# Performance work log

Hardware: AMD Instinct MI355X
Metric: run time of the kernel (lower is better)

## Reference

```python
import jax, jax.numpy as jnp
import numpy as np

NUM_FEATURES = 1024
NUM_SAMPLES = 32768
BATCH = 4096
TEMP = 0.05
EPS = 1e-12


def setup_inputs() -> dict:
    key = jax.random.key(0)
    k1, k2, k3, k4 = jax.random.split(key, 4)
    inputs = jax.random.normal(k1, (BATCH, NUM_FEATURES), dtype=jnp.float32)
    targets = jax.random.randint(k2, (BATCH,), 0, NUM_SAMPLES, dtype=jnp.int64)
    corrected_targets = jax.random.randint(k3, (BATCH,), 0, NUM_SAMPLES, dtype=jnp.int64)
    # memory bank: buffer is zeros-initialized in torch, but in practice it is
    # filled with L2-normalized cluster centroids before use; emulate that.
    feats = jax.random.normal(k4, (NUM_SAMPLES, NUM_FEATURES), dtype=jnp.float32)
    feats = feats / jnp.linalg.norm(feats, axis=1, keepdims=True)
    return {"inputs": inputs, "targets": targets,
            "corrected_targets": corrected_targets, "features": feats}


def reference(inputs, targets, corrected_targets, features):
    # F.normalize(inputs, dim=1)
    x = inputs / jnp.maximum(jnp.linalg.norm(inputs, axis=1, keepdims=True), EPS)
    # CM.forward: inputs @ features.T, then / temp
    logits = jnp.einsum('bd,nd->bn', x, features) / TEMP  # [B, N]
    # F.cross_entropy(logits, corrected_targets, reduction='mean')
    logp = jax.nn.log_softmax(logits, axis=1)
    nll = -jnp.take_along_axis(logp, corrected_targets[:, None], axis=1)[:, 0]
    return jnp.mean(nll)
```

## Files before the change

kernel.cpp:

```cpp
#include <hip/hip_runtime.h>
#include <stdint.h>

#define B_ROWS 4096
#define N_FEAT 32768
#define K_DIM  1024
#define BM 256
#define BN 256
#define NT2 (N_FEAT / BN)
#define NKT (K_DIM / 64)

typedef __attribute__((ext_vector_type(8))) short bf16x8;
typedef __attribute__((ext_vector_type(4))) float f32x4;
typedef __attribute__((address_space(1))) unsigned char ga_u8;
typedef __attribute__((address_space(3))) unsigned char lds_u8;

__device__ inline unsigned short f2bf(float f) {
  union { float f; unsigned u; } v; v.f = f;
  unsigned r = v.u + 0x7FFF + ((v.u >> 16) & 1);
  return (unsigned short)(r >> 16);
}
__device__ inline float bf2f(unsigned short u) {
  union { unsigned u; float f; } v; v.u = ((unsigned)u) << 16;
  return v.f;
}

__global__ void k_prep(const float* __restrict__ in, unsigned short* __restrict__ xbf,
                       const float* __restrict__ f, unsigned short* __restrict__ fbf) {
  int bid = blockIdx.x;
  int t = threadIdx.x;
  if (bid < B_ROWS) {
    int row = bid;
    float4 v = reinterpret_cast<const float4*>(in + (size_t)row * K_DIM)[t];
    float ssq = v.x * v.x + v.y * v.y + v.z * v.z + v.w * v.w;
    #pragma unroll
    for (int d = 1; d < 64; d <<= 1) ssq += __shfl_xor(ssq, d);
    __shared__ float sm[4];
    if ((t & 63) == 0) sm[t >> 6] = ssq;
    __syncthreads();
    float nrm = sqrtf(sm[0] + sm[1] + sm[2] + sm[3]);
    float inv = 1.0f / fmaxf(nrm, 1e-12f);
    ushort4 o;
    o.x = f2bf(v.x * inv); o.y = f2bf(v.y * inv);
    o.z = f2bf(v.z * inv); o.w = f2bf(v.w * inv);
    reinterpret_cast<ushort4*>(xbf + (size_t)row * K_DIM)[t] = o;
  } else {
    const long n4 = (long)N_FEAT * K_DIM / 4;
    long i = (long)(bid - B_ROWS) * 256 + t;
    const long stride = 2048L * 256;
    for (; i < n4; i += stride) {
      float4 v = reinterpret_cast<const float4*>(f)[i];
      ushort4 o;
      o.x = f2bf(v.x); o.y = f2bf(v.y); o.z = f2bf(v.z); o.w = f2bf(v.w);
      reinterpret_cast<ushort4*>(fbf)[i] = o;
    }
  }
}

__global__ void k_tgt(const unsigned short* __restrict__ xbf,
                      const unsigned short* __restrict__ fbf,
                      const int* __restrict__ tgt, float* __restrict__ out) {
  int row = blockIdx.x * 4 + (threadIdx.x >> 6);
  int lane = threadIdx.x & 63;
  int t = tgt[row];
  const uint4* xa = reinterpret_cast<const uint4*>(xbf + (size_t)row * K_DIM + lane * 16);
  const uint4* fa = reinterpret_cast<const uint4*>(fbf + (size_t)t * K_DIM + lane * 16);
  float s = 0.f;
  #pragma unroll
  for (int j = 0; j < 2; ++j) {
    uint4 av = xa[j], fv = fa[j];
    const unsigned* ap = &av.x;
    const unsigned* fp = &fv.x;
    #pragma unroll
    for (int q = 0; q < 4; ++q) {
      s += bf2f((unsigned short)(ap[q] & 0xffff)) * bf2f((unsigned short)(fp[q] & 0xffff));
      s += bf2f((unsigned short)(ap[q] >> 16)) * bf2f((unsigned short)(fp[q] >> 16));
    }
  }
  #pragma unroll
  for (int d = 1; d < 64; d <<= 1) s += __shfl_xor(s, d);
  if (lane == 0) out[row] = s * 20.0f;
}


#define XSTR(s) STR(s)
#define STR(s) #s
#define WAITV(N)  asm volatile("s_waitcnt vmcnt(" XSTR(N) ")" ::: "memory")
#define LGKM0     do { asm volatile("s_waitcnt lgkmcnt(0)" ::: "memory"); __builtin_amdgcn_sched_barrier(0); } while(0)
#define BAR       __builtin_amdgcn_s_barrier()
#define SCHED0    __builtin_amdgcn_sched_barrier(0)
#define PRIO1     __builtin_amdgcn_s_setprio(1)
#define PRIO0     __builtin_amdgcn_s_setprio(0)

__launch_bounds__(512, 2)
__global__ void k_gemm8(const unsigned short* __restrict__ xbf,
                        const unsigned short* __restrict__ fbf,
                        float* __restrict__ m_part, float* __restrict__ l_part) {
  __shared__ __align__(16) char lds_all[131072];
  char* ldsc = lds_all;

  int tid = threadIdx.x;
  int lane = tid & 63;
  int wid = tid >> 6;
  int wr = wid >> 2;
  int wc = wid & 3;
  int r15 = lane & 15;
  int g = lane >> 4;

  int bid = blockIdx.x;
  int swz = (bid & 7) * 256 + (bid >> 3);
  int mt = swz >> 7;
  int nt = swz & 127;
  int mBase = mt * BM, nBase = nt * BN;

  int lswz = ((g ^ ((r15 >> 1) & 3)) << 4);
  int aRow = (wr * 128 + r15) * 64 + lswz;
  int bRow = (wc * 64 + r15) * 64 + lswz + 32768;

  int stRow = wid * 32 + (lane >> 2);
  int src_cb = (((lane & 3) ^ ((lane >> 3) & 3)) << 4);
  const char* srcA = (const char*)xbf + (size_t)(mBase + stRow) * (K_DIM * 2) + src_cb;
  const char* srcB = (const char*)fbf + (size_t)(nBase + stRow) * (K_DIM * 2) + src_cb;

#define STAGE(BSEL_, MAT, KH, T) do { \
    const char* gsrc = ((MAT) ? srcB : srcA) + (T) * 128 + (KH) * 64; \
    char* ldst = ldsc + (BSEL_) * 65536 + (MAT) * 32768 + (KH) * 16384 + wid * 2048; \
    __builtin_amdgcn_global_load_lds((const ga_u8*)gsrc, (lds_u8*)ldst, 16, 0, 0); \
    __builtin_amdgcn_global_load_lds((const ga_u8*)(gsrc + 32768), (lds_u8*)(ldst + 1024), 16, 0, 0); \
  } while(0)

#define PHASE(T, KH, DOST, SB, SKH, ST, VMN) do { \
    char* bufc = ldsc + ((T) & 1) * 65536 + (KH) * 16384; \
    _Pragma("unroll") \
    for (int fm = 0; fm < 8; ++fm) \
      a[fm] = *reinterpret_cast<const bf16x8*>(bufc + aRow + fm * 1024); \
    _Pragma("unroll") \
    for (int fn = 0; fn < 4; ++fn) \
      b[fn] = *reinterpret_cast<const bf16x8*>(bufc + bRow + fn * 1024); \
    if (DOST) { STAGE(SB, 0, SKH, ST); STAGE(SB, 1, SKH, ST); } \
    WAITV(VMN); \
    BAR; LGKM0; PRIO1; \
    _Pragma("unroll") \
    for (int fm = 0; fm < 8; ++fm) \
      _Pragma("unroll") \
      for (int fn = 0; fn < 4; ++fn) \
        acc[fm][fn] = __builtin_amdgcn_mfma_f32_16x16x32_bf16(a[fm], b[fn], acc[fm][fn], 0, 0, 0); \
    PRIO0; BAR; SCHED0; \
  } while(0)

  f32x4 acc[8][4];
  #pragma unroll
  for (int i = 0; i < 8; ++i)
    #pragma unroll
    for (int j = 0; j < 4; ++j)
      acc[i][j] = (f32x4){0.f, 0.f, 0.f, 0.f};
  bf16x8 a[8], b[4];

  STAGE(0, 0, 0, 0); STAGE(0, 1, 0, 0);
  STAGE(0, 0, 1, 0); STAGE(0, 1, 1, 0);
  STAGE(1, 0, 0, 1); STAGE(1, 1, 0, 1);
  WAITV(8);
  BAR; SCHED0;

  for (int t = 0; t < NKT - 2; ++t) {
    PHASE(t, 0, 1, (t + 1) & 1, 1, t + 1, 8);
    PHASE(t, 1, 1, t & 1,       0, t + 2, 8);
  }
  PHASE(14, 0, 1, 1, 1, 15, 8);
  PHASE(14, 1, 0, 0, 0, 0, 4);
  PHASE(15, 0, 0, 0, 0, 0, 0);
  PHASE(15, 1, 0, 0, 0, 0, 0);

  asm volatile("s_waitcnt vmcnt(0) lgkmcnt(0)" ::: "memory");
  __syncthreads();
  float* sm_m = (float*)lds_all;
  float* sm_l = (float*)(lds_all + 4096);

  #pragma unroll
  for (int mf = 0; mf < 8; ++mf)
    #pragma unroll
    for (int fn = 0; fn < 4; ++fn)
      acc[mf][fn] = acc[mf][fn] * 20.0f;

  #pragma unroll
  for (int mf = 0; mf < 8; ++mf) {
    #pragma unroll
    for (int reg = 0; reg < 4; ++reg) {
      float mx = -1e30f;
      #pragma unroll
      for (int fn = 0; fn < 4; ++fn) mx = fmaxf(mx, acc[mf][fn][reg]);
      mx = fmaxf(mx, __shfl_xor(mx, 1));
      mx = fmaxf(mx, __shfl_xor(mx, 2));
      mx = fmaxf(mx, __shfl_xor(mx, 4));
      mx = fmaxf(mx, __shfl_xor(mx, 8));
      float sum = 0.f;
      #pragma unroll
      for (int fn = 0; fn < 4; ++fn) sum += __expf(acc[mf][fn][reg] - mx);
      sum += __shfl_xor(sum, 1);
      sum += __shfl_xor(sum, 2);
      sum += __shfl_xor(sum, 4);
      sum += __shfl_xor(sum, 8);
      if ((lane & 15) == 0) {
        int r = wr * 128 + mf * 16 + (lane >> 4) * 4 + reg;
        sm_m[wc * 256 + r] = mx;
        sm_l[wc * 256 + r] = sum;
      }
    }
  }
  __syncthreads();
  if (tid < 256) {
    float M = sm_m[tid], L = sm_l[tid];
    #pragma unroll
    for (int w = 1; w < 4; ++w) {
      float mo = sm_m[w * 256 + tid], lo = sm_l[w * 256 + tid];
      float mn = fmaxf(M, mo);
      L = L * __expf(M - mn) + lo * __expf(mo - mn);
      M = mn;
    }
    size_t idx = (size_t)(mBase + tid) * NT2 + nt;
    m_part[idx] = M;
    l_part[idx] = L;
  }
}

__global__ void k_comb(const float* __restrict__ m_part, const float* __restrict__ l_part,
                       const float* __restrict__ tgt_logit, float* __restrict__ out) {
  int row = blockIdx.x;
  int lane = threadIdx.x;
  size_t base = (size_t)row * NT2;
  float m = m_part[base + lane];
  float l = l_part[base + lane];
  float m2 = m_part[base + 64 + lane];
  float l2 = l_part[base + 64 + lane];
  float mn = fmaxf(m, m2);
  l = l * __expf(m - mn) + l2 * __expf(m2 - mn);
  m = mn;
  #pragma unroll
  for (int d = 1; d < 64; d <<= 1) {
    float mo = __shfl_xor(m, d);
    float lo = __shfl_xor(l, d);
    float mx = fmaxf(m, mo);
    l = l * __expf(m - mx) + lo * __expf(mo - mx);
    m = mx;
  }
  if (lane == 0) {
    float nll = m + __logf(l) - tgt_logit[row];
    atomicAdd(out, nll * (1.0f / B_ROWS));
  }
}

extern "C" void kernel_launch(void* const* d_in, const int* in_sizes, int n_in,
                              void* d_out, int out_size, void* d_ws, size_t ws_size,
                              hipStream_t stream) {
  const float* inputs = (const float*)d_in[0];
  const int* ctgt = (const int*)d_in[2];
  const float* feats = (const float*)d_in[3];
  float* out = (float*)d_out;

  char* ws = (char*)d_ws;
  unsigned short* xbf = (unsigned short*)ws;
  unsigned short* fbf = (unsigned short*)(ws + (8ull << 20));
  float* m_part = (float*)(ws + (72ull << 20));
  float* l_part = (float*)(ws + (74ull << 20));
  float* tgt_logit = (float*)(ws + (76ull << 20));

  hipMemsetAsync(out, 0, sizeof(float), stream);
  k_prep<<<B_ROWS + 2048, 256, 0, stream>>>(inputs, xbf, feats, fbf);
  k_tgt<<<B_ROWS / 4, 256, 0, stream>>>(xbf, fbf, ctgt, tgt_logit);
  k_gemm8<<<(B_ROWS / BM) * (N_FEAT / BN), 512, 0, stream>>>(xbf, fbf, m_part, l_part);
  k_comb<<<B_ROWS, 64, 0, stream>>>(m_part, l_part, tgt_logit, out);
}
```

Before: 599.0 us.

## Use 5-slot LDS ring with register double-buffered fragments in GEMM

Reworks the GEMM main loop into a 5-slot LDS ring of 32-wide K chunks. The next chunk's fragments are loaded into a second register set while MFMAs run on the current one, which removes one of the two barriers per phase and overlaps LDS reads with compute. LDS use grows to 160KB, which may drop occupancy to one block per CU, and the doubled fragment registers add register pressure. It also widens the feature-conversion grid and replaces the memset-plus-atomicAdd mean with a deterministic per-row store followed by a single-block reduction kernel.

```diff
diff --git a/kernel.cpp b/kernel.cpp
--- a/kernel.cpp
+++ b/kernel.cpp
@@ -7,7 +7,6 @@
 #define BM 256
 #define BN 256
 #define NT2 (N_FEAT / BN)
-#define NKT (K_DIM / 64)
 
 typedef __attribute__((ext_vector_type(8))) short bf16x8;
 typedef __attribute__((ext_vector_type(4))) float f32x4;
@@ -46,7 +45,7 @@
   } else {
     const long n4 = (long)N_FEAT * K_DIM / 4;
     long i = (long)(bid - B_ROWS) * 256 + t;
-    const long stride = 2048L * 256;
+    const long stride = 8192L * 256;
     for (; i < n4; i += stride) {
       float4 v = reinterpret_cast<const float4*>(f)[i];
       ushort4 o;
@@ -84,8 +83,8 @@
 
 #define XSTR(s) STR(s)
 #define STR(s) #s
-#define WAITV(N)  asm volatile("s_waitcnt vmcnt(" XSTR(N) ")" ::: "memory")
-#define LGKM0     do { asm volatile("s_waitcnt lgkmcnt(0)" ::: "memory"); __builtin_amdgcn_sched_barrier(0); } while(0)
+#define WAITVN(N) asm volatile("s_waitcnt vmcnt(" XSTR(N) ")" ::: "memory")
+#define LGKMN(N)  do { asm volatile("s_waitcnt lgkmcnt(" XSTR(N) ")" ::: "memory"); __builtin_amdgcn_sched_barrier(0); } while(0)
 #define BAR       __builtin_amdgcn_s_barrier()
 #define SCHED0    __builtin_amdgcn_sched_barrier(0)
 #define PRIO1     __builtin_amdgcn_s_setprio(1)
@@ -95,7 +94,7 @@
 __global__ void k_gemm8(const unsigned short* __restrict__ xbf,
                         const unsigned short* __restrict__ fbf,
                         float* __restrict__ m_part, float* __restrict__ l_part) {
-  __shared__ __align__(16) char lds_all[131072];
+  __shared__ __align__(16) char lds_all[163840];
   char* ldsc = lds_all;
 
   int tid = threadIdx.x;
@@ -113,39 +112,54 @@
   int mBase = mt * BM, nBase = nt * BN;
 
   int lswz = ((g ^ ((r15 >> 1) & 3)) << 4);
-  int aRow = (wr * 128 + r15) * 64 + lswz;
-  int bRow = (wc * 64 + r15) * 64 + lswz + 32768;
+  int aOff = (wr * 128 + r15) * 64 + lswz;
+  int bOff = 16384 + (wc * 64 + r15) * 64 + lswz;
 
   int stRow = wid * 32 + (lane >> 2);
   int src_cb = (((lane & 3) ^ ((lane >> 3) & 3)) << 4);
   const char* srcA = (const char*)xbf + (size_t)(mBase + stRow) * (K_DIM * 2) + src_cb;
   const char* srcB = (const char*)fbf + (size_t)(nBase + stRow) * (K_DIM * 2) + src_cb;
 
-#define STAGE(BSEL_, MAT, KH, T) do { \
-    const char* gsrc = ((MAT) ? srcB : srcA) + (T) * 128 + (KH) * 64; \
-    char* ldst = ldsc + (BSEL_) * 65536 + (MAT) * 32768 + (KH) * 16384 + wid * 2048; \
-    __builtin_amdgcn_global_load_lds((const ga_u8*)gsrc, (lds_u8*)ldst, 16, 0, 0); \
-    __builtin_amdgcn_global_load_lds((const ga_u8*)(gsrc + 32768), (lds_u8*)(ldst + 1024), 16, 0, 0); \
+#define STAGE5(SLOT, H) do { \
+    const char* gA = srcA + (H) * 64; \
+    char* dA = ldsc + (SLOT) * 32768 + wid * 2048; \
+    __builtin_amdgcn_global_load_lds((const ga_u8*)gA, (lds_u8*)dA, 16, 0, 0); \
+    __builtin_amdgcn_global_load_lds((const ga_u8*)(gA + 32768), (lds_u8*)(dA + 1024), 16, 0, 0); \
+    const char* gB = srcB + (H) * 64; \
+    char* dB = ldsc + (SLOT) * 32768 + 16384 + wid * 2048; \
+    __builtin_amdgcn_global_load_lds((const ga_u8*)gB, (lds_u8*)dB, 16, 0, 0); \
+    __builtin_amdgcn_global_load_lds((const ga_u8*)(gB + 32768), (lds_u8*)(dB + 1024), 16, 0, 0); \
   } while(0)
 
-#define PHASE(T, KH, DOST, SB, SKH, ST, VMN) do { \
-    char* bufc = ldsc + ((T) & 1) * 65536 + (KH) * 16384; \
+#define LDF(AA, BB, SLOT) do { \
+    char* sb = ldsc + (SLOT) * 32768; \
     _Pragma("unroll") \
     for (int fm = 0; fm < 8; ++fm) \
-      a[fm] = *reinterpret_cast<const bf16x8*>(bufc + aRow + fm * 1024); \
+      AA[fm] = *reinterpret_cast<const bf16x8*>(sb + aOff + fm * 1024); \
     _Pragma("unroll") \
     for (int fn = 0; fn < 4; ++fn) \
-      b[fn] = *reinterpret_cast<const bf16x8*>(bufc + bRow + fn * 1024); \
-    if (DOST) { STAGE(SB, 0, SKH, ST); STAGE(SB, 1, SKH, ST); } \
-    WAITV(VMN); \
-    BAR; LGKM0; PRIO1; \
+      BB[fn] = *reinterpret_cast<const bf16x8*>(sb + bOff + fn * 1024); \
+  } while(0)
+
+#define MM5(AA, BB) do { \
     _Pragma("unroll") \
     for (int fm = 0; fm < 8; ++fm) \
       _Pragma("unroll") \
       for (int fn = 0; fn < 4; ++fn) \
-        acc[fm][fn] = __builtin_amdgcn_mfma_f32_16x16x32_bf16(a[fm], b[fn], acc[fm][fn], 0, 0, 0); \
-    PRIO0; BAR; SCHED0; \
+        acc[fm][fn] = __builtin_amdgcn_mfma_f32_16x16x32_bf16(AA[fm], BB[fn], acc[fm][fn], 0, 0, 0); \
   } while(0)
+
+#define PHASE5(SNXT, SSTG, DOST, DOLD, VM, LG, ACUR, BCUR, ANXT, BNXT, H) do { \
+    if (DOST) { STAGE5(SSTG, H); } \
+    WAITVN(VM); \
+    if (DOLD) { LDF(ANXT, BNXT, SNXT); } \
+    LGKMN(LG); \
+    PRIO1; MM5(ACUR, BCUR); PRIO0; \
+    BAR; SCHED0; \
+  } while(0)
+
+#define PH_E(SNXT, SSTG, H) PHASE5(SNXT, SSTG, 1, 1, 8, 12, a0, b0, a1, b1, H)
+#define PH_O(SNXT, SSTG, H) PHASE5(SNXT, SSTG, 1, 1, 8, 12, a1, b1, a0, b0, H)
 
   f32x4 acc[8][4];
   #pragma unroll
@@ -153,22 +167,23 @@
     #pragma unroll
     for (int j = 0; j < 4; ++j)
       acc[i][j] = (f32x4){0.f, 0.f, 0.f, 0.f};
-  bf16x8 a[8], b[4];
-
-  STAGE(0, 0, 0, 0); STAGE(0, 1, 0, 0);
-  STAGE(0, 0, 1, 0); STAGE(0, 1, 1, 0);
-  STAGE(1, 0, 0, 1); STAGE(1, 1, 0, 1);
-  WAITV(8);
+  bf16x8 a0[8], b0[4], a1[8], b1[4];
+
+  STAGE5(0, 0); STAGE5(1, 1); STAGE5(2, 2); STAGE5(3, 3);
+  WAITVN(8);
   BAR; SCHED0;
-
-  for (int t = 0; t < NKT - 2; ++t) {
-    PHASE(t, 0, 1, (t + 1) & 1, 1, t + 1, 8);
-    PHASE(t, 1, 1, t & 1,       0, t + 2, 8);
-  }
-  PHASE(14, 0, 1, 1, 1, 15, 8);
-  PHASE(14, 1, 0, 0, 0, 0, 4);
-  PHASE(15, 0, 0, 0, 0, 0, 0);
-  PHASE(15, 1, 0, 0, 0, 0, 0);
+  LDF(a0, b0, 0);
+
+  PH_E(1, 4, 4);   PH_O(2, 0, 5);   PH_E(3, 1, 6);   PH_O(4, 2, 7);   PH_E(0, 3, 8);
+  PH_O(1, 4, 9);   PH_E(2, 0, 10);  PH_O(3, 1, 11);  PH_E(4, 2, 12);  PH_O(0, 3, 13);
+  PH_E(1, 4, 14);  PH_O(2, 0, 15);  PH_E(3, 1, 16);  PH_O(4, 2, 17);  PH_E(0, 3, 18);
+  PH_O(1, 4, 19);  PH_E(2, 0, 20);  PH_O(3, 1, 21);  PH_E(4, 2, 22);  PH_O(0, 3, 23);
+  PH_E(1, 4, 24);  PH_O(2, 0, 25);  PH_E(3, 1, 26);  PH_O(4, 2, 27);  PH_E(0, 3, 28);
+  PH_O(1, 4, 29);  PH_E(2, 0, 30);  PH_O(3, 1, 31);
+  PHASE5(4, 0, 0, 1, 4, 12, a0, b0, a1, b1, 0);
+  PHASE5(0, 0, 0, 1, 0, 12, a1, b1, a0, b0, 0);
+  PHASE5(1, 0, 0, 1, 0, 12, a0, b0, a1, b1, 0);
+  PHASE5(0, 0, 0, 0, 0, 0,  a1, b1, a0, b0, 0);
 
   asm volatile("s_waitcnt vmcnt(0) lgkmcnt(0)" ::: "memory");
   __syncthreads();
@@ -223,7 +238,7 @@
 }
 
 __global__ void k_comb(const float* __restrict__ m_part, const float* __restrict__ l_part,
-                       const float* __restrict__ tgt_logit, float* __restrict__ out) {
+                       const float* __restrict__ tgt_logit, float* __restrict__ nll) {
   int row = blockIdx.x;
   int lane = threadIdx.x;
   size_t base = (size_t)row * NT2;
@@ -242,9 +257,24 @@
     l = l * __expf(m - mx) + lo * __expf(mo - mx);
     m = mx;
   }
-  if (lane == 0) {
-    float nll = m + __logf(l) - tgt_logit[row];
-    atomicAdd(out, nll * (1.0f / B_ROWS));
+  if (lane == 0) nll[row] = m + __logf(l) - tgt_logit[row];
+}
+
+__global__ void k_mean(const float* __restrict__ nll, float* __restrict__ out) {
+  int t = threadIdx.x;
+  float s = 0.f;
+  #pragma unroll
+  for (int i = 0; i < 4; ++i) s += nll[t + i * 1024];
+  #pragma unroll
+  for (int d = 1; d < 64; d <<= 1) s += __shfl_xor(s, d);
+  __shared__ float sm[16];
+  if ((t & 63) == 0) sm[t >> 6] = s;
+  __syncthreads();
+  if (t == 0) {
+    float tot = 0.f;
+    #pragma unroll
+    for (int w = 0; w < 16; ++w) tot += sm[w];
+    out[0] = tot * (1.0f / B_ROWS);
   }
 }
 
@@ -262,10 +292,11 @@
   float* m_part = (float*)(ws + (72ull << 20));
   float* l_part = (float*)(ws + (74ull << 20));
   float* tgt_logit = (float*)(ws + (76ull << 20));
-
-  hipMemsetAsync(out, 0, sizeof(float), stream);
-  k_prep<<<B_ROWS + 2048, 256, 0, stream>>>(inputs, xbf, feats, fbf);
+  float* nll = (float*)(ws + (76ull << 20) + (64ull << 10));
+
+  k_prep<<<B_ROWS + 8192, 256, 0, stream>>>(inputs, xbf, feats, fbf);
   k_tgt<<<B_ROWS / 4, 256, 0, stream>>>(xbf, fbf, ctgt, tgt_logit);
   k_gemm8<<<(B_ROWS / BM) * (N_FEAT / BN), 512, 0, stream>>>(xbf, fbf, m_part, l_part);
-  k_comb<<<B_ROWS, 64, 0, stream>>>(m_part, l_part, tgt_logit, out);
-}
+  k_comb<<<B_ROWS, 64, 0, stream>>>(m_part, l_part, tgt_logit, nll);
+  k_mean<<<1, 1024, 0, stream>>>(nll, out);
+}
```

New measurement: 524.6 us. 1.14x faster.
